# Performance work log

Hardware: AMD Instinct MI355X
Metric: run time of the kernel (lower is better)

The kernel has to match this reference:

```python
import jax, jax.numpy as jnp
import numpy as np

D = 1024
H = 16
HD = D // H

def setup_inputs() -> dict:
    key = jax.random.key(0)
    ks = jax.random.split(key, 5)
    scale = 1.0 / np.sqrt(D)
    x = jax.random.normal(ks[0], (2, 2048, D), dtype=jnp.float32)
    W_qkv = jax.random.uniform(ks[1], (D, 3 * D), minval=-scale, maxval=scale, dtype=jnp.float32)
    b_qkv = jax.random.uniform(ks[2], (3 * D,), minval=-scale, maxval=scale, dtype=jnp.float32)
    W_out = jax.random.uniform(ks[3], (D, D), minval=-scale, maxval=scale, dtype=jnp.float32)
    b_out = jax.random.uniform(ks[4], (D,), minval=-scale, maxval=scale, dtype=jnp.float32)
    return {"x": x, "W_qkv": W_qkv, "b_qkv": b_qkv, "W_out": W_out, "b_out": b_out}

def reference(x, W_qkv, b_qkv, W_out, b_out):
    B, S, _ = x.shape
    qkv = x @ W_qkv + b_qkv  # [B,S,3D]
    qkv = qkv.reshape(B, S, 3, H, HD).transpose(2, 0, 3, 1, 4)  # [3,B,H,S,HD]
    q, k, v = qkv[0], qkv[1], qkv[2]
    scores = jnp.einsum('bhsd,bhtd->bhst', q, k) / jnp.sqrt(jnp.float32(HD))
    probs = jax.nn.softmax(scores, axis=-1)
    attn = jnp.einsum('bhst,bhtd->bhsd', probs, v)  # [B,H,S,HD]
    attn = attn.transpose(0, 2, 1, 3).reshape(B, S, D)
    return attn @ W_out + b_out
```

## Files before the change

kernel.cpp:

```cpp
#include <hip/hip_runtime.h>


typedef short bf16x8 __attribute__((ext_vector_type(8)));
typedef float f32x4 __attribute__((ext_vector_type(4)));

#define MFMA32(a, b, c) __builtin_amdgcn_mfma_f32_16x16x32_bf16(a, b, c, 0, 0, 0)

__device__ __forceinline__ unsigned short f2bf(float f) {
  unsigned u = __float_as_uint(f);
  u = (u + 0x7fffu + ((u >> 16) & 1u)) >> 16;
  return (unsigned short)u;
}
__device__ __forceinline__ unsigned pack_bf2(float lo, float hi) {
  unsigned a = __float_as_uint(lo) + 0x8000u;
  unsigned b = __float_as_uint(hi) + 0x8000u;
  return __builtin_amdgcn_perm(b, a, 0x07060302);
}
__device__ __forceinline__ void load_lds16(const unsigned short* g, unsigned short* l) {
  __builtin_amdgcn_global_load_lds(
      (const __attribute__((address_space(1))) void*)g,
      (__attribute__((address_space(3))) void*)l, 16, 0, 0);
}

__global__ __launch_bounds__(256) void prep(
    const float* __restrict__ x, unsigned short* __restrict__ x_bf,
    const float* __restrict__ W_qkv, unsigned short* __restrict__ Wqkv_t,
    const float* __restrict__ W_out, unsigned short* __restrict__ Wout_t)
{
  const int tid = threadIdx.x;
  if (blockIdx.z == 2) {
    const int bid = blockIdx.y * 48 + blockIdx.x;
    const int n = 4096 * 1024;
    for (int i = bid * 2048 + tid * 8; i < n; i += 768 * 2048) {
      float4 f0 = *(const float4*)(x + i);
      float4 f1 = *(const float4*)(x + i + 4);
      union { unsigned short u[8]; uint4 v; } pk;
      pk.u[0] = f2bf(f0.x); pk.u[1] = f2bf(f0.y); pk.u[2] = f2bf(f0.z); pk.u[3] = f2bf(f0.w);
      pk.u[4] = f2bf(f1.x); pk.u[5] = f2bf(f1.y); pk.u[6] = f2bf(f1.z); pk.u[7] = f2bf(f1.w);
      *(uint4*)(x_bf + i) = pk.v;
    }
    return;
  }
  const float* in = (blockIdx.z == 0) ? W_qkv : W_out;
  unsigned short* out = (blockIdx.z == 0) ? Wqkv_t : Wout_t;
  const int R = 1024;
  const int C = (blockIdx.z == 0) ? 3072 : 1024;
  const int c0 = blockIdx.x * 64;
  if (c0 >= C) return;
  __shared__ float tile[64][65];
  const int r0 = blockIdx.y * 64;
  {
    const int rr = tid >> 4;
    const int cc = (tid & 15) * 4;
#pragma unroll
    for (int it = 0; it < 4; ++it) {
      float4 f = *(const float4*)&in[(size_t)(r0 + rr + 16 * it) * C + c0 + cc];
      tile[rr + 16 * it][cc + 0] = f.x;
      tile[rr + 16 * it][cc + 1] = f.y;
      tile[rr + 16 * it][cc + 2] = f.z;
      tile[rr + 16 * it][cc + 3] = f.w;
    }
  }
  __syncthreads();
  {
    const int cr = tid >> 2;
    const int rk = (tid & 3) * 16;
    union { unsigned short u[16]; uint4 v[2]; } pk;
#pragma unroll
    for (int j = 0; j < 16; ++j) pk.u[j] = f2bf(tile[rk + j][cr]);
    uint4* dst = (uint4*)&out[(size_t)(c0 + cr) * R + r0 + rk];
    dst[0] = pk.v[0];
    dst[1] = pk.v[1];
  }
}

template <int MODE>
__global__ __launch_bounds__(256) void gemm_mfma(
    const unsigned short* __restrict__ A,
    const unsigned short* __restrict__ Bt,
    const float* __restrict__ bias,
    void* __restrict__ Cout, unsigned short* __restrict__ vT,
    int M, int N, int K, int ldc)
{
  __shared__ unsigned short As[128][32];
  __shared__ unsigned short Bs[128][32];
  const int tid = threadIdx.x;
  const int wave = tid >> 6, lane = tid & 63;
  const int l16 = lane & 15, quad = lane >> 4;
  const int m0 = blockIdx.y * 128, n0 = blockIdx.x * 128;
  const int wm = (wave & 1) * 64, wn = (wave >> 1) * 64;
  const int lr = lane >> 2;
  const int lc = (lane & 3) * 8;

  f32x4 acc[4][4] = {};

  for (int k0 = 0; k0 < K; k0 += 32) {
    __syncthreads();
    load_lds16(&A [(size_t)(m0 + 16 * wave + lr) * K + k0 + lc],      &As[16 * wave][0]);
    load_lds16(&A [(size_t)(m0 + 64 + 16 * wave + lr) * K + k0 + lc], &As[64 + 16 * wave][0]);
    load_lds16(&Bt[(size_t)(n0 + 16 * wave + lr) * K + k0 + lc],      &Bs[16 * wave][0]);
    load_lds16(&Bt[(size_t)(n0 + 64 + 16 * wave + lr) * K + k0 + lc], &Bs[64 + 16 * wave][0]);
    __syncthreads();

    bf16x8 af[4], bfr[4];
#pragma unroll
    for (int mi = 0; mi < 4; ++mi)
      af[mi] = *(const bf16x8*)&As[wm + 16 * mi + l16][quad * 8];
#pragma unroll
    for (int ni = 0; ni < 4; ++ni)
      bfr[ni] = *(const bf16x8*)&Bs[wn + 16 * ni + l16][quad * 8];
#pragma unroll
    for (int mi = 0; mi < 4; ++mi)
#pragma unroll
      for (int ni = 0; ni < 4; ++ni)
        acc[mi][ni] = __builtin_amdgcn_mfma_f32_16x16x32_bf16(
            af[mi], bfr[ni], acc[mi][ni], 0, 0, 0);
  }

  const float SCQ = 0.18033688f;
#pragma unroll
  for (int ni = 0; ni < 4; ++ni) {
    const int colb = n0 + wn + 16 * ni;
    const int col = colb + l16;
    const float bv = bias[col];
    if (MODE == 0) {
#pragma unroll
      for (int mi = 0; mi < 4; ++mi)
#pragma unroll
        for (int i = 0; i < 4; ++i) {
          const int row = m0 + wm + 16 * mi + quad * 4 + i;
          ((float*)Cout)[(size_t)row * ldc + col] = acc[mi][ni][i] + bv;
        }
    } else if (colb < 1024) {
#pragma unroll
      for (int mi = 0; mi < 4; ++mi)
#pragma unroll
        for (int i = 0; i < 4; ++i) {
          const int row = m0 + wm + 16 * mi + quad * 4 + i;
          ((unsigned short*)Cout)[(size_t)row * ldc + col] = f2bf((acc[mi][ni][i] + bv) * SCQ);
        }
    } else if (colb < 2048) {
#pragma unroll
      for (int mi = 0; mi < 4; ++mi)
#pragma unroll
        for (int i = 0; i < 4; ++i) {
          const int row = m0 + wm + 16 * mi + quad * 4 + i;
          ((unsigned short*)Cout)[(size_t)row * ldc + col] = f2bf(acc[mi][ni][i] + bv);
        }
    } else {
      const int h = (col - 2048) >> 6, d = col & 63;
#pragma unroll
      for (int mi = 0; mi < 4; ++mi) {
        const int row = m0 + wm + 16 * mi + quad * 4;
        const int bb = row >> 11, t = row & 2047;
        unsigned short* dst = &vT[((size_t)(bb * 16 + h) * 64 + d) * 2048 + t];
        *(unsigned*)(dst)     = pack_bf2(acc[mi][ni][0] + bv, acc[mi][ni][1] + bv);
        *(unsigned*)(dst + 2) = pack_bf2(acc[mi][ni][2] + bv, acc[mi][ni][3] + bv);
      }
    }
  }
}

__global__ __launch_bounds__(256, 2) void attn_mfma(
    const unsigned short* __restrict__ qk,
    const unsigned short* __restrict__ vT,
    unsigned short* __restrict__ attn_out)
{
  __shared__ unsigned short Ks[2][4096];
  __shared__ unsigned short Vs[2][4096];

  const int tid = threadIdx.x;
  const int wave = tid >> 6, lane = tid & 63;
  const int l16 = lane & 15, quad = lane >> 4;
  const int bh = blockIdx.y, b = bh >> 4, h = bh & 15;
  const int s0 = blockIdx.x * 128 + wave * 32;

  const unsigned short* qb = qk + (size_t)(b * 2048) * 2048 + h * 64;
  const unsigned short* kb = qb + 1024;
  const unsigned short* vb = vT + (size_t)bh * 64 * 2048;

  const int srow = lane >> 3;
  const int schunk = ((lane & 7) ^ srow) * 8;
  const int r0a = wave * 16;
  const unsigned short* kg0 = kb + (size_t)(r0a + srow) * 2048 + schunk;
  const unsigned short* kg1 = kg0 + (size_t)8 * 2048;
  const unsigned short* vg0 = vb + (size_t)(r0a + srow) * 2048 + schunk;
  const unsigned short* vg1 = vg0 + (size_t)8 * 2048;
  const int wd0 = r0a * 64 + lane * 8;
  const int wd1 = (r0a + 8) * 64 + lane * 8;

  uint4 kr0 = *(const uint4*)(kg0);
  uint4 kr1 = *(const uint4*)(kg1);
  uint4 vr0 = *(const uint4*)(vg0);
  uint4 vr1 = *(const uint4*)(vg1);
  *(uint4*)&Ks[0][wd0] = kr0;  *(uint4*)&Ks[0][wd1] = kr1;
  *(uint4*)&Vs[0][wd0] = vr0;  *(uint4*)&Vs[0][wd1] = vr1;
  kr0 = *(const uint4*)(kg0 + (size_t)64 * 2048);
  kr1 = *(const uint4*)(kg1 + (size_t)64 * 2048);
  vr0 = *(const uint4*)(vg0 + 64);
  vr1 = *(const uint4*)(vg1 + 64);

  bf16x8 qf[2][2];
#pragma unroll
  for (int mt = 0; mt < 2; ++mt)
#pragma unroll
    for (int ks = 0; ks < 2; ++ks)
      qf[mt][ks] = *(const bf16x8*)&qb[(size_t)(s0 + 16 * mt + l16) * 2048 + 32 * ks + quad * 8];

  f32x4 O[2][4] = {};
  f32x4 lacc[2] = {};
  const bf16x8 ones8 = {(short)0x3F80, (short)0x3F80, (short)0x3F80, (short)0x3F80,
                        (short)0x3F80, (short)0x3F80, (short)0x3F80, (short)0x3F80};
  const int sw = l16 & 7;

  __syncthreads();

  for (int it = 0; it < 32; ++it) {
    const int cur = it & 1;

    bf16x8 kf[4][2];
#pragma unroll
    for (int nt = 0; nt < 4; ++nt) {
      const int rb = (16 * nt + l16) * 64;
      kf[nt][0] = *(const bf16x8*)&Ks[cur][rb + ((quad ^ sw) * 8)];
      kf[nt][1] = *(const bf16x8*)&Ks[cur][rb + (((4 + quad) ^ sw) * 8)];
    }

    f32x4 sf[4][2];
#pragma unroll
    for (int nt = 0; nt < 4; ++nt)
#pragma unroll
      for (int mt = 0; mt < 2; ++mt) {
        f32x4 c = {0.0f, 0.0f, 0.0f, 0.0f};
        c = __builtin_amdgcn_mfma_f32_16x16x32_bf16(kf[nt][0], qf[mt][0], c, 0, 0, 0);
        c = __builtin_amdgcn_mfma_f32_16x16x32_bf16(kf[nt][1], qf[mt][1], c, 0, 0, 0);
        sf[nt][mt] = c;
      }

    if (it < 31) {
      *(uint4*)&Ks[cur ^ 1][wd0] = kr0;
      *(uint4*)&Ks[cur ^ 1][wd1] = kr1;
      *(uint4*)&Vs[cur ^ 1][wd0] = vr0;
      *(uint4*)&Vs[cur ^ 1][wd1] = vr1;
      if (it < 30) {
        const size_t ko = (size_t)(it + 2) * 64 * 2048;
        kr0 = *(const uint4*)(kg0 + ko);
        kr1 = *(const uint4*)(kg1 + ko);
        vr0 = *(const uint4*)(vg0 + (it + 2) * 64);
        vr1 = *(const uint4*)(vg1 + (it + 2) * 64);
      }
    }

    bf16x8 vf[4][2];
#pragma unroll
    for (int nd = 0; nd < 4; ++nd) {
      const int rb = (16 * nd + l16) * 64;
      vf[nd][0] = *(const bf16x8*)&Vs[cur][rb + ((quad ^ sw) * 8)];
      vf[nd][1] = *(const bf16x8*)&Vs[cur][rb + (((4 + quad) ^ sw) * 8)];
    }

    bf16x8 pB[2][2];
#pragma unroll
    for (int mt = 0; mt < 2; ++mt)
#pragma unroll
      for (int c = 0; c < 2; ++c) {
        const f32x4 sa = sf[2 * c][mt];
        const f32x4 sb = sf[2 * c + 1][mt];
        unsigned X = pack_bf2(__builtin_amdgcn_exp2f(sa[0]), __builtin_amdgcn_exp2f(sa[1]));
        unsigned Y = pack_bf2(__builtin_amdgcn_exp2f(sa[2]), __builtin_amdgcn_exp2f(sa[3]));
        unsigned Z = pack_bf2(__builtin_amdgcn_exp2f(sb[0]), __builtin_amdgcn_exp2f(sb[1]));
        unsigned W = pack_bf2(__builtin_amdgcn_exp2f(sb[2]), __builtin_amdgcn_exp2f(sb[3]));
        asm("v_permlane32_swap_b32 %0, %1" : "+v"(X), "+v"(Z));
        asm("v_permlane16_swap_b32 %0, %1" : "+v"(X), "+v"(Z));
        asm("v_permlane32_swap_b32 %0, %1" : "+v"(Y), "+v"(W));
        asm("v_permlane16_swap_b32 %0, %1" : "+v"(Y), "+v"(W));
        union { unsigned u[4]; bf16x8 v; } pk;
        pk.u[0] = X; pk.u[1] = Y; pk.u[2] = Z; pk.u[3] = W;
        pB[mt][c] = pk.v;
      }

#pragma unroll
    for (int c = 0; c < 2; ++c)
#pragma unroll
      for (int mt = 0; mt < 2; ++mt) {
        lacc[mt] = MFMA32(ones8, pB[mt][c], lacc[mt]);
#pragma unroll
        for (int nd = 0; nd < 4; ++nd)
          O[mt][nd] = MFMA32(vf[nd][c], pB[mt][c], O[mt][nd]);
      }

    __syncthreads();
  }

#pragma unroll
  for (int mt = 0; mt < 2; ++mt) {
    const float inv = 1.0f / lacc[mt][0];
    const size_t row = (size_t)(b * 2048 + s0 + 16 * mt + l16);
#pragma unroll
    for (int nd = 0; nd < 4; ++nd) {
      uint2 w;
      w.x = pack_bf2(O[mt][nd][0] * inv, O[mt][nd][1] * inv);
      w.y = pack_bf2(O[mt][nd][2] * inv, O[mt][nd][3] * inv);
      *(uint2*)&attn_out[row * 1024 + h * 64 + 16 * nd + quad * 4] = w;
    }
  }
}

extern "C" void kernel_launch(void* const* d_in, const int* in_sizes, int n_in,
                              void* d_out, int out_size, void* d_ws, size_t ws_size,
                              hipStream_t stream) {
  const float* x     = (const float*)d_in[0];
  const float* W_qkv = (const float*)d_in[1];
  const float* b_qkv = (const float*)d_in[2];
  const float* W_out = (const float*)d_in[3];
  const float* b_out = (const float*)d_in[4];
  float* out = (float*)d_out;

  char* ws = (char*)d_ws;
  const size_t MB = 1048576;
  unsigned short* Wout_t = (unsigned short*)(ws);
  unsigned short* qk_bf  = (unsigned short*)(ws + 2 * MB);
  unsigned short* vT     = (unsigned short*)(ws + 18 * MB);
  unsigned short* attn_b = (unsigned short*)(ws + 26 * MB);
  unsigned short* x_bf   = (unsigned short*)(ws + 34 * MB);
  unsigned short* Wqkv_t = (unsigned short*)(ws + 42 * MB);

  prep<<<dim3(48, 16, 3), 256, 0, stream>>>(x, x_bf, W_qkv, Wqkv_t, W_out, Wout_t);

  gemm_mfma<1><<<dim3(24, 32), 256, 0, stream>>>(x_bf, Wqkv_t, b_qkv, qk_bf, vT,
                                                 4096, 3072, 1024, 2048);
  attn_mfma<<<dim3(16, 32), 256, 0, stream>>>(qk_bf, vT, attn_b);
  gemm_mfma<0><<<dim3(8, 32), 256, 0, stream>>>(attn_b, Wout_t, b_out, out, nullptr,
                                                4096, 1024, 1024, 1024);
}
```

Measured before the change: 194.5 us.

## Split attention key loop across two wave groups with LDS reduction

Doubles the attention block to 512 threads, with the two halves of the block each processing half of the key/value sequence in separate LDS buffers. The partial unnormalized outputs and row sums from the second half are written to shared memory and added by the first half before normalization and store. This halves the serial loop length per wave and raises waves in flight, at the cost of doubled LDS per block, an extra reduction step and tighter register limits from the launch bounds.

```diff
diff --git a/kernel.cpp b/kernel.cpp
--- a/kernel.cpp
+++ b/kernel.cpp
@@ -161,19 +161,24 @@
   }
 }
 
-__global__ __launch_bounds__(256, 2) void attn_mfma(
+__global__ __launch_bounds__(512, 4) void attn_mfma(
     const unsigned short* __restrict__ qk,
     const unsigned short* __restrict__ vT,
     unsigned short* __restrict__ attn_out)
 {
-  __shared__ unsigned short Ks[2][4096];
-  __shared__ unsigned short Vs[2][4096];
+  __shared__ __align__(16) char smraw[65536];
+  unsigned short (*Ks)[2][4096] = (unsigned short (*)[2][4096])smraw;
+  unsigned short (*Vs)[2][4096] = (unsigned short (*)[2][4096])(smraw + 32768);
+  float* Ox = (float*)smraw;
+  float* lX = (float*)(smraw + 32768);
 
   const int tid = threadIdx.x;
   const int wave = tid >> 6, lane = tid & 63;
+  const int wq = wave & 3, half = wave >> 2;
   const int l16 = lane & 15, quad = lane >> 4;
   const int bh = blockIdx.y, b = bh >> 4, h = bh & 15;
-  const int s0 = blockIdx.x * 128 + wave * 32;
+  const int s0 = blockIdx.x * 128 + wq * 32;
+  const int tbase = half * 1024;
 
   const unsigned short* qb = qk + (size_t)(b * 2048) * 2048 + h * 64;
   const unsigned short* kb = qb + 1024;
@@ -181,10 +186,10 @@
 
   const int srow = lane >> 3;
   const int schunk = ((lane & 7) ^ srow) * 8;
-  const int r0a = wave * 16;
-  const unsigned short* kg0 = kb + (size_t)(r0a + srow) * 2048 + schunk;
+  const int r0a = wq * 16;
+  const unsigned short* kg0 = kb + (size_t)(tbase + r0a + srow) * 2048 + schunk;
   const unsigned short* kg1 = kg0 + (size_t)8 * 2048;
-  const unsigned short* vg0 = vb + (size_t)(r0a + srow) * 2048 + schunk;
+  const unsigned short* vg0 = vb + (size_t)(r0a + srow) * 2048 + tbase + schunk;
   const unsigned short* vg1 = vg0 + (size_t)8 * 2048;
   const int wd0 = r0a * 64 + lane * 8;
   const int wd1 = (r0a + 8) * 64 + lane * 8;
@@ -193,8 +198,8 @@
   uint4 kr1 = *(const uint4*)(kg1);
   uint4 vr0 = *(const uint4*)(vg0);
   uint4 vr1 = *(const uint4*)(vg1);
-  *(uint4*)&Ks[0][wd0] = kr0;  *(uint4*)&Ks[0][wd1] = kr1;
-  *(uint4*)&Vs[0][wd0] = vr0;  *(uint4*)&Vs[0][wd1] = vr1;
+  *(uint4*)&Ks[half][0][wd0] = kr0;  *(uint4*)&Ks[half][0][wd1] = kr1;
+  *(uint4*)&Vs[half][0][wd0] = vr0;  *(uint4*)&Vs[half][0][wd1] = vr1;
   kr0 = *(const uint4*)(kg0 + (size_t)64 * 2048);
   kr1 = *(const uint4*)(kg1 + (size_t)64 * 2048);
   vr0 = *(const uint4*)(vg0 + 64);
@@ -215,15 +220,15 @@
 
   __syncthreads();
 
-  for (int it = 0; it < 32; ++it) {
+  for (int it = 0; it < 16; ++it) {
     const int cur = it & 1;
 
     bf16x8 kf[4][2];
 #pragma unroll
     for (int nt = 0; nt < 4; ++nt) {
       const int rb = (16 * nt + l16) * 64;
-      kf[nt][0] = *(const bf16x8*)&Ks[cur][rb + ((quad ^ sw) * 8)];
-      kf[nt][1] = *(const bf16x8*)&Ks[cur][rb + (((4 + quad) ^ sw) * 8)];
+      kf[nt][0] = *(const bf16x8*)&Ks[half][cur][rb + ((quad ^ sw) * 8)];
+      kf[nt][1] = *(const bf16x8*)&Ks[half][cur][rb + (((4 + quad) ^ sw) * 8)];
     }
 
     f32x4 sf[4][2];
@@ -237,12 +242,12 @@
         sf[nt][mt] = c;
       }
 
-    if (it < 31) {
-      *(uint4*)&Ks[cur ^ 1][wd0] = kr0;
-      *(uint4*)&Ks[cur ^ 1][wd1] = kr1;
-      *(uint4*)&Vs[cur ^ 1][wd0] = vr0;
-      *(uint4*)&Vs[cur ^ 1][wd1] = vr1;
-      if (it < 30) {
+    if (it < 15) {
+      *(uint4*)&Ks[half][cur ^ 1][wd0] = kr0;
+      *(uint4*)&Ks[half][cur ^ 1][wd1] = kr1;
+      *(uint4*)&Vs[half][cur ^ 1][wd0] = vr0;
+      *(uint4*)&Vs[half][cur ^ 1][wd1] = vr1;
+      if (it < 14) {
         const size_t ko = (size_t)(it + 2) * 64 * 2048;
         kr0 = *(const uint4*)(kg0 + ko);
         kr1 = *(const uint4*)(kg1 + ko);
@@ -255,8 +260,8 @@
 #pragma unroll
     for (int nd = 0; nd < 4; ++nd) {
       const int rb = (16 * nd + l16) * 64;
-      vf[nd][0] = *(const bf16x8*)&Vs[cur][rb + ((quad ^ sw) * 8)];
-      vf[nd][1] = *(const bf16x8*)&Vs[cur][rb + (((4 + quad) ^ sw) * 8)];
+      vf[nd][0] = *(const bf16x8*)&Vs[half][cur][rb + ((quad ^ sw) * 8)];
+      vf[nd][1] = *(const bf16x8*)&Vs[half][cur][rb + (((4 + quad) ^ sw) * 8)];
     }
 
     bf16x8 pB[2][2];
@@ -292,16 +297,31 @@
     __syncthreads();
   }
 
-#pragma unroll
-  for (int mt = 0; mt < 2; ++mt) {
-    const float inv = 1.0f / lacc[mt][0];
-    const size_t row = (size_t)(b * 2048 + s0 + 16 * mt + l16);
-#pragma unroll
-    for (int nd = 0; nd < 4; ++nd) {
-      uint2 w;
-      w.x = pack_bf2(O[mt][nd][0] * inv, O[mt][nd][1] * inv);
-      w.y = pack_bf2(O[mt][nd][2] * inv, O[mt][nd][3] * inv);
-      *(uint2*)&attn_out[row * 1024 + h * 64 + 16 * nd + quad * 4] = w;
+  if (half) {
+#pragma unroll
+    for (int mt = 0; mt < 2; ++mt) {
+      lX[(wq * 2 + mt) * 64 + lane] = lacc[mt][0];
+#pragma unroll
+      for (int nd = 0; nd < 4; ++nd)
+        *(f32x4*)&Ox[(((wq * 2 + mt) * 4 + nd) * 64 + lane) * 4] = O[mt][nd];
+    }
+  }
+  __syncthreads();
+  if (!half) {
+#pragma unroll
+    for (int mt = 0; mt < 2; ++mt) {
+      const float lsum = lacc[mt][0] + lX[(wq * 2 + mt) * 64 + lane];
+      const float inv = 1.0f / lsum;
+      const size_t row = (size_t)(b * 2048 + s0 + 16 * mt + l16);
+#pragma unroll
+      for (int nd = 0; nd < 4; ++nd) {
+        const f32x4 o2 = *(const f32x4*)&Ox[(((wq * 2 + mt) * 4 + nd) * 64 + lane) * 4];
+        const f32x4 oo = O[mt][nd] + o2;
+        uint2 w;
+        w.x = pack_bf2(oo[0] * inv, oo[1] * inv);
+        w.y = pack_bf2(oo[2] * inv, oo[3] * inv);
+        *(uint2*)&attn_out[row * 1024 + h * 64 + 16 * nd + quad * 4] = w;
+      }
     }
   }
 }
@@ -329,7 +349,7 @@
 
   gemm_mfma<1><<<dim3(24, 32), 256, 0, stream>>>(x_bf, Wqkv_t, b_qkv, qk_bf, vT,
                                                  4096, 3072, 1024, 2048);
-  attn_mfma<<<dim3(16, 32), 256, 0, stream>>>(qk_bf, vT, attn_b);
+  attn_mfma<<<dim3(16, 32), 512, 0, stream>>>(qk_bf, vT, attn_b);
   gemm_mfma<0><<<dim3(8, 32), 256, 0, stream>>>(attn_b, Wout_t, b_out, out, nullptr,
                                                 4096, 1024, 1024, 1024);
 }
```

After: 205.6 us. +5.7%, slower.

## Software-pipeline attention PV step with 4-stage LDS ring; narrow out-proj GEMM tiles

Applied to the files above, without the earlier changes.

The attention loop now keeps four K/V LDS buffers and defers each iteration's P·V MFMA to the next iteration. This lets the exp/pack work for the current tile overlap with the previous tile's MFMAs, and the loads are prefetched one stage deeper. The output-projection GEMM gets a templated N tile of 64, which doubles its grid to 512 blocks to raise occupancy on the small problem. The permlane swaps now use compiler builtins when available. The cost is double the LDS in the attention kernel, which may limit how many blocks fit per CU, plus more registers held live across iterations.

```diff
diff --git a/kernel.cpp b/kernel.cpp
--- a/kernel.cpp
+++ b/kernel.cpp
@@ -3,6 +3,7 @@
 
 typedef short bf16x8 __attribute__((ext_vector_type(8)));
 typedef float f32x4 __attribute__((ext_vector_type(4)));
+typedef unsigned uint2v __attribute__((ext_vector_type(2)));
 
 #define MFMA32(a, b, c) __builtin_amdgcn_mfma_f32_16x16x32_bf16(a, b, c, 0, 0, 0)
 
@@ -21,6 +22,26 @@
       (const __attribute__((address_space(1))) void*)g,
       (__attribute__((address_space(3))) void*)l, 16, 0, 0);
 }
+
+#if __has_builtin(__builtin_amdgcn_permlane32_swap)
+__device__ __forceinline__ void pl32_swap(unsigned& a, unsigned& b) {
+  uint2v r = __builtin_amdgcn_permlane32_swap(a, b, false, false);
+  a = r[0]; b = r[1];
+}
+__device__ __forceinline__ void pl16_swap(unsigned& a, unsigned& b) {
+  uint2v r = __builtin_amdgcn_permlane16_swap(a, b, false, false);
+  a = r[0]; b = r[1];
+}
+#else
+__device__ __forceinline__ void pl32_swap(unsigned& a, unsigned& b) {
+  asm volatile("s_nop 1\n\tv_permlane32_swap_b32 %0, %1\n\ts_nop 1"
+               : "+v"(a), "+v"(b));
+}
+__device__ __forceinline__ void pl16_swap(unsigned& a, unsigned& b) {
+  asm volatile("s_nop 1\n\tv_permlane16_swap_b32 %0, %1\n\ts_nop 1"
+               : "+v"(a), "+v"(b));
+}
+#endif
 
 __global__ __launch_bounds__(256) void prep(
     const float* __restrict__ x, unsigned short* __restrict__ x_bf,
@@ -74,7 +95,7 @@
   }
 }
 
-template <int MODE>
+template <int MODE, int NB>
 __global__ __launch_bounds__(256) void gemm_mfma(
     const unsigned short* __restrict__ A,
     const unsigned short* __restrict__ Bt,
@@ -82,44 +103,46 @@
     void* __restrict__ Cout, unsigned short* __restrict__ vT,
     int M, int N, int K, int ldc)
 {
+  constexpr int NI = NB / 32;
   __shared__ unsigned short As[128][32];
-  __shared__ unsigned short Bs[128][32];
+  __shared__ unsigned short Bs[NB][32];
   const int tid = threadIdx.x;
   const int wave = tid >> 6, lane = tid & 63;
   const int l16 = lane & 15, quad = lane >> 4;
-  const int m0 = blockIdx.y * 128, n0 = blockIdx.x * 128;
-  const int wm = (wave & 1) * 64, wn = (wave >> 1) * 64;
+  const int m0 = blockIdx.y * 128, n0 = blockIdx.x * NB;
+  const int wm = (wave & 1) * 64, wn = (wave >> 1) * (NB / 2);
   const int lr = lane >> 2;
   const int lc = (lane & 3) * 8;
 
-  f32x4 acc[4][4] = {};
+  f32x4 acc[4][NI] = {};
 
   for (int k0 = 0; k0 < K; k0 += 32) {
     __syncthreads();
     load_lds16(&A [(size_t)(m0 + 16 * wave + lr) * K + k0 + lc],      &As[16 * wave][0]);
     load_lds16(&A [(size_t)(m0 + 64 + 16 * wave + lr) * K + k0 + lc], &As[64 + 16 * wave][0]);
     load_lds16(&Bt[(size_t)(n0 + 16 * wave + lr) * K + k0 + lc],      &Bs[16 * wave][0]);
-    load_lds16(&Bt[(size_t)(n0 + 64 + 16 * wave + lr) * K + k0 + lc], &Bs[64 + 16 * wave][0]);
+    if constexpr (NB == 128)
+      load_lds16(&Bt[(size_t)(n0 + 64 + 16 * wave + lr) * K + k0 + lc], &Bs[64 + 16 * wave][0]);
     __syncthreads();
 
-    bf16x8 af[4], bfr[4];
+    bf16x8 af[4], bfr[NI];
 #pragma unroll
     for (int mi = 0; mi < 4; ++mi)
       af[mi] = *(const bf16x8*)&As[wm + 16 * mi + l16][quad * 8];
 #pragma unroll
-    for (int ni = 0; ni < 4; ++ni)
+    for (int ni = 0; ni < NI; ++ni)
       bfr[ni] = *(const bf16x8*)&Bs[wn + 16 * ni + l16][quad * 8];
 #pragma unroll
     for (int mi = 0; mi < 4; ++mi)
 #pragma unroll
-      for (int ni = 0; ni < 4; ++ni)
+      for (int ni = 0; ni < NI; ++ni)
         acc[mi][ni] = __builtin_amdgcn_mfma_f32_16x16x32_bf16(
             af[mi], bfr[ni], acc[mi][ni], 0, 0, 0);
   }
 
   const float SCQ = 0.18033688f;
 #pragma unroll
-  for (int ni = 0; ni < 4; ++ni) {
+  for (int ni = 0; ni < NI; ++ni) {
     const int colb = n0 + wn + 16 * ni;
     const int col = colb + l16;
     const float bv = bias[col];
@@ -166,8 +189,8 @@
     const unsigned short* __restrict__ vT,
     unsigned short* __restrict__ attn_out)
 {
-  __shared__ unsigned short Ks[2][4096];
-  __shared__ unsigned short Vs[2][4096];
+  __shared__ unsigned short Ks[4][4096];
+  __shared__ unsigned short Vs[4][4096];
 
   const int tid = threadIdx.x;
   const int wave = tid >> 6, lane = tid & 63;
@@ -199,6 +222,12 @@
   kr1 = *(const uint4*)(kg1 + (size_t)64 * 2048);
   vr0 = *(const uint4*)(vg0 + 64);
   vr1 = *(const uint4*)(vg1 + 64);
+  *(uint4*)&Ks[1][wd0] = kr0;  *(uint4*)&Ks[1][wd1] = kr1;
+  *(uint4*)&Vs[1][wd0] = vr0;  *(uint4*)&Vs[1][wd1] = vr1;
+  kr0 = *(const uint4*)(kg0 + (size_t)128 * 2048);
+  kr1 = *(const uint4*)(kg1 + (size_t)128 * 2048);
+  vr0 = *(const uint4*)(vg0 + 128);
+  vr1 = *(const uint4*)(vg1 + 128);
 
   bf16x8 qf[2][2];
 #pragma unroll
@@ -209,6 +238,7 @@
 
   f32x4 O[2][4] = {};
   f32x4 lacc[2] = {};
+  bf16x8 pB[2][2];
   const bf16x8 ones8 = {(short)0x3F80, (short)0x3F80, (short)0x3F80, (short)0x3F80,
                         (short)0x3F80, (short)0x3F80, (short)0x3F80, (short)0x3F80};
   const int sw = l16 & 7;
@@ -216,7 +246,7 @@
   __syncthreads();
 
   for (int it = 0; it < 32; ++it) {
-    const int cur = it & 1;
+    const int cur = it & 3;
 
     bf16x8 kf[4][2];
 #pragma unroll
@@ -237,29 +267,41 @@
         sf[nt][mt] = c;
       }
 
-    if (it < 31) {
-      *(uint4*)&Ks[cur ^ 1][wd0] = kr0;
-      *(uint4*)&Ks[cur ^ 1][wd1] = kr1;
-      *(uint4*)&Vs[cur ^ 1][wd0] = vr0;
-      *(uint4*)&Vs[cur ^ 1][wd1] = vr1;
-      if (it < 30) {
-        const size_t ko = (size_t)(it + 2) * 64 * 2048;
+    if (it < 30) {
+      const int nb = (it + 2) & 3;
+      *(uint4*)&Ks[nb][wd0] = kr0;
+      *(uint4*)&Ks[nb][wd1] = kr1;
+      *(uint4*)&Vs[nb][wd0] = vr0;
+      *(uint4*)&Vs[nb][wd1] = vr1;
+      if (it < 29) {
+        const size_t ko = (size_t)(it + 3) * 64 * 2048;
         kr0 = *(const uint4*)(kg0 + ko);
         kr1 = *(const uint4*)(kg1 + ko);
-        vr0 = *(const uint4*)(vg0 + (it + 2) * 64);
-        vr1 = *(const uint4*)(vg1 + (it + 2) * 64);
-      }
-    }
-
-    bf16x8 vf[4][2];
-#pragma unroll
-    for (int nd = 0; nd < 4; ++nd) {
-      const int rb = (16 * nd + l16) * 64;
-      vf[nd][0] = *(const bf16x8*)&Vs[cur][rb + ((quad ^ sw) * 8)];
-      vf[nd][1] = *(const bf16x8*)&Vs[cur][rb + (((4 + quad) ^ sw) * 8)];
-    }
-
-    bf16x8 pB[2][2];
+        vr0 = *(const uint4*)(vg0 + (it + 3) * 64);
+        vr1 = *(const uint4*)(vg1 + (it + 3) * 64);
+      }
+    }
+
+    if (it > 0) {
+      const int pv = (it + 3) & 3;
+      bf16x8 vf[4][2];
+#pragma unroll
+      for (int nd = 0; nd < 4; ++nd) {
+        const int rb = (16 * nd + l16) * 64;
+        vf[nd][0] = *(const bf16x8*)&Vs[pv][rb + ((quad ^ sw) * 8)];
+        vf[nd][1] = *(const bf16x8*)&Vs[pv][rb + (((4 + quad) ^ sw) * 8)];
+      }
+#pragma unroll
+      for (int c = 0; c < 2; ++c)
+#pragma unroll
+        for (int mt = 0; mt < 2; ++mt) {
+          lacc[mt] = MFMA32(ones8, pB[mt][c], lacc[mt]);
+#pragma unroll
+          for (int nd = 0; nd < 4; ++nd)
+            O[mt][nd] = MFMA32(vf[nd][c], pB[mt][c], O[mt][nd]);
+        }
+    }
+
 #pragma unroll
     for (int mt = 0; mt < 2; ++mt)
 #pragma unroll
@@ -270,15 +312,26 @@
         unsigned Y = pack_bf2(__builtin_amdgcn_exp2f(sa[2]), __builtin_amdgcn_exp2f(sa[3]));
         unsigned Z = pack_bf2(__builtin_amdgcn_exp2f(sb[0]), __builtin_amdgcn_exp2f(sb[1]));
         unsigned W = pack_bf2(__builtin_amdgcn_exp2f(sb[2]), __builtin_amdgcn_exp2f(sb[3]));
-        asm("v_permlane32_swap_b32 %0, %1" : "+v"(X), "+v"(Z));
-        asm("v_permlane16_swap_b32 %0, %1" : "+v"(X), "+v"(Z));
-        asm("v_permlane32_swap_b32 %0, %1" : "+v"(Y), "+v"(W));
-        asm("v_permlane16_swap_b32 %0, %1" : "+v"(Y), "+v"(W));
+        pl32_swap(X, Z);
+        pl16_swap(X, Z);
+        pl32_swap(Y, W);
+        pl16_swap(Y, W);
         union { unsigned u[4]; bf16x8 v; } pk;
         pk.u[0] = X; pk.u[1] = Y; pk.u[2] = Z; pk.u[3] = W;
         pB[mt][c] = pk.v;
       }
 
+    __syncthreads();
+  }
+
+  {
+    bf16x8 vf[4][2];
+#pragma unroll
+    for (int nd = 0; nd < 4; ++nd) {
+      const int rb = (16 * nd + l16) * 64;
+      vf[nd][0] = *(const bf16x8*)&Vs[3][rb + ((quad ^ sw) * 8)];
+      vf[nd][1] = *(const bf16x8*)&Vs[3][rb + (((4 + quad) ^ sw) * 8)];
+    }
 #pragma unroll
     for (int c = 0; c < 2; ++c)
 #pragma unroll
@@ -288,8 +341,6 @@
         for (int nd = 0; nd < 4; ++nd)
           O[mt][nd] = MFMA32(vf[nd][c], pB[mt][c], O[mt][nd]);
       }
-
-    __syncthreads();
   }
 
 #pragma unroll
@@ -327,9 +378,9 @@
 
   prep<<<dim3(48, 16, 3), 256, 0, stream>>>(x, x_bf, W_qkv, Wqkv_t, W_out, Wout_t);
 
-  gemm_mfma<1><<<dim3(24, 32), 256, 0, stream>>>(x_bf, Wqkv_t, b_qkv, qk_bf, vT,
-                                                 4096, 3072, 1024, 2048);
+  gemm_mfma<1, 128><<<dim3(24, 32), 256, 0, stream>>>(x_bf, Wqkv_t, b_qkv, qk_bf, vT,
+                                                      4096, 3072, 1024, 2048);
   attn_mfma<<<dim3(16, 32), 256, 0, stream>>>(qk_bf, vT, attn_b);
-  gemm_mfma<0><<<dim3(8, 32), 256, 0, stream>>>(attn_b, Wout_t, b_out, out, nullptr,
-                                                4096, 1024, 1024, 1024);
-}
+  gemm_mfma<0, 64><<<dim3(16, 32), 256, 0, stream>>>(attn_b, Wout_t, b_out, out, nullptr,
+                                                     4096, 1024, 1024, 1024);
+}
```

Result: faster. 190.5 us (-2.0%).
